# Optimization experiments

Hardware: AMD Instinct MI355X
Metric: run time of the kernel (lower is better)

The kernel has to match this reference:

```python
import jax, jax.numpy as jnp
import numpy as np

# ---- db6 filter bank (pywt conventions) ----
_REC_LO = np.array([0.11154074335008017, 0.4946238903983854, 0.7511339080215775,
                    0.3152503517092432, -0.22626469396516913, -0.12976686756709563,
                    0.09750160558707936, 0.02752286553001629, -0.031582039318031156,
                    0.0005538422009938016, 0.004777257511010651, -0.00107730108499558],
                   dtype=np.float32)
_REC_HI = _REC_LO[::-1].copy(); _REC_HI[1::2] *= -1.0          # qmf(rec_lo)
_DEC_LO = _REC_LO[::-1].copy()
_DEC_HI = _REC_HI[::-1].copy()
L = 12          # filter length
LEVEL = 8       # J
# pytorch_wavelets cross-correlates with dec[::-1] == true conv with dec.
# lax.conv_general_dilated is correlation, so analysis kernels = dec[::-1] = rec filters.
ANA = jnp.asarray(np.stack([_REC_LO, _REC_HI])[:, None, :])     # [2,1,L]
SYN = jnp.asarray(np.stack([_DEC_LO, _DEC_HI])[None, :, :])     # [1,2,L]


def dwt1d(x, J):
    """Multi-level DWT, mode='symmetric'. x: [B,C,N] -> (yl [B,C,m], [yh1..yhJ])."""
    B, C, N = x.shape
    lo = x.reshape(B * C, 1, N)
    highs = []
    for _ in range(J):
        n = lo.shape[-1]
        outlen = (n + L - 1) // 2                    # pywt dwt_coeff_len
        p = 2 * (outlen - 1) - n + L
        xp = jnp.pad(lo, ((0, 0), (0, 0), (p // 2, (p + 1) // 2)), mode='symmetric')
        y = jax.lax.conv_general_dilated(xp, ANA, (2,), 'VALID',
                                         dimension_numbers=('NCH', 'OIH', 'NCH'))
        lo = y[:, :1]
        highs.append(y[:, 1:].reshape(B, C, outlen))
    return lo.reshape(B, C, -1), highs


def idwt1d(yl, yhs):
    """Inverse of dwt1d. yl: [B,C,m], yhs list (level1..levelJ)."""
    B, C, _ = yl.shape
    lo = yl.reshape(B * C, 1, -1)
    pad = L - 1 - (L - 2)                            # torch convT padding L-2 -> lax pad 1
    for h in yhs[::-1]:
        h = h.reshape(B * C, 1, -1)
        if lo.shape[-1] > h.shape[-1]:               # 'unpad' extra sample
            lo = lo[..., :h.shape[-1]]
        xh = jnp.concatenate([lo, h], axis=1)        # [BC,2,n]
        lo = jax.lax.conv_general_dilated(xh, SYN, (1,), [(pad, pad)],
                                          lhs_dilation=(2,),
                                          dimension_numbers=('NCH', 'OIH', 'NCH'))
    return lo.reshape(B, C, -1)


def wno_forward(x, fc0_w, fc0_b, w1, w2, cw, cb, fc1_w, fc1_b, fc2_w, fc2_b):
    B, s, _ = x.shape
    grid = jnp.broadcast_to(jnp.linspace(0.0, 1.0, s, dtype=x.dtype)[None, :, None], (B, s, 1))
    v = jnp.concatenate([x, grid], axis=-1) @ fc0_w + fc0_b     # [B,s,W]
    v = v.transpose(0, 2, 1)                                     # [B,W,s]
    n_layers = w1.shape[0]
    for i in range(n_layers):
        yl, yhs = dwt1d(v, LEVEL)
        yl = jnp.einsum('bix,iox->box', yl, w1[i])               # mix approx coeffs
        yhs[-1] = jnp.einsum('bix,iox->box', yhs[-1], w2[i])     # mix finest-level detail
        x1 = idwt1d(yl, yhs)
        x2 = jnp.einsum('bis,io->bos', v, cw[i]) + cb[i][None, :, None]  # 1x1 conv
        v = x1 + x2
        if i < n_layers - 1:
            v = jax.nn.gelu(v, approximate=False)
    v = v.transpose(0, 2, 1)
    v = jax.nn.gelu(v @ fc1_w + fc1_b, approximate=False)
    return v @ fc2_w + fc2_b                                     # [B,s,1]


def setup_inputs() -> dict:
    key = jax.random.key(0)
    B, S, W, NL = 32, 8192, 64, 4
    n = S
    for _ in range(LEVEL):
        n = (n + L - 1) // 2
    modes = n                                                    # 42
    ks = jax.random.split(key, 12)
    scale = 1.0 / (W * W)
    return {
        'x': jax.random.normal(ks[0], (B, S, 1), jnp.float32),
        'fc0_w': jax.random.normal(ks[1], (2, W), jnp.float32) * 0.5,
        'fc0_b': jax.random.normal(ks[2], (W,), jnp.float32) * 0.1,
        'w1': scale * jax.random.uniform(ks[3], (NL, W, W, modes), jnp.float32),
        'w2': scale * jax.random.uniform(ks[4], (NL, W, W, modes), jnp.float32),
        'cw': jax.random.normal(ks[5], (NL, W, W), jnp.float32) * (1.0 / np.sqrt(W)),
        'cb': jax.random.normal(ks[6], (NL, W), jnp.float32) * 0.05,
        'fc1_w': jax.random.normal(ks[7], (W, 128), jnp.float32) * (1.0 / np.sqrt(W)),
        'fc1_b': jax.random.normal(ks[8], (128,), jnp.float32) * 0.05,
        'fc2_w': jax.random.normal(ks[9], (128, 1), jnp.float32) * (1.0 / np.sqrt(128.0)),
        'fc2_b': jax.random.normal(ks[10], (1,), jnp.float32) * 0.05,
    }


def reference(x, fc0_w, fc0_b, w1, w2, cw, cb, fc1_w, fc1_b, fc2_w, fc2_b):
    return wno_forward(x, fc0_w, fc0_b, w1, w2, cw, cb, fc1_w, fc1_b, fc2_w, fc2_b)
```

## Files before the change

kernel.cpp:

```cpp
#include <hip/hip_runtime.h>
#include <cmath>

#define BC 2048
#define S_LEN 8192
#define MODES 42
#define HTOT 8248
#define LO_STR 1036

static constexpr float C_LO[12] = {
  0.11154074335008017f, 0.4946238903983854f, 0.7511339080215775f,
  0.3152503517092432f, -0.22626469396516913f, -0.12976686756709563f,
  0.09750160558707936f, 0.02752286553001629f, -0.031582039318031156f,
  0.0005538422009938016f, 0.004777257511010651f, -0.00107730108499558f };

__device__ __forceinline__ float rec_lo_c(int k){ return C_LO[k]; }
__device__ __forceinline__ float rec_hi_c(int k){ float v = C_LO[11-k]; return (k&1)? -v : v; }
__device__ __forceinline__ float dec_lo_c(int k){ return C_LO[11-k]; }
__device__ __forceinline__ float dec_hi_c(int k){ float v = C_LO[k];    return (k&1)?  v : -v; }

__device__ __forceinline__ float erf_fast(float x){
  float ax = fabsf(x);
  float t  = __fdividef(1.0f, 1.0f + 0.3275911f * ax);
  float p  = ((((1.061405429f * t - 1.453152027f) * t) + 1.421413741f) * t - 0.284496736f) * t + 0.254829592f;
  float y  = 1.0f - p * t * __expf(-ax * ax);
  return copysignf(y, x);
}
__device__ __forceinline__ float gelu_f(float x){
  return 0.5f * x * (1.0f + erf_fast(x * 0.70710678118654752440f));
}

__device__ __forceinline__ int reflect_i(int t, int n){
  t = (t < 0) ? (-1 - t) : t;
  t = (t >= n) ? (2 * n - 1 - t) : t;
  return t;
}

__device__ __forceinline__ unsigned short bf16_rn(float x){
  unsigned int b = __float_as_uint(x);
  b += 0x7FFF + ((b >> 16) & 1);
  return (unsigned short)(b >> 16);
}
__device__ __forceinline__ float bf16_to_f(unsigned short h){
  return __uint_as_float(((unsigned int)h) << 16);
}

typedef short  v8s __attribute__((ext_vector_type(8)));
typedef float  v4f __attribute__((ext_vector_type(4)));
typedef unsigned short u16;

__device__ __forceinline__ void ld3f4(float* w, const float* s){
  *(float4*)&w[0] = *(const float4*)&s[0];
  *(float4*)&w[4] = *(const float4*)&s[4];
  *(float4*)&w[8] = *(const float4*)&s[8];
}
__device__ __forceinline__ void ld5f4(float* w, const float* s){
  *(float4*)&w[0]  = *(const float4*)&s[0];
  *(float4*)&w[4]  = *(const float4*)&s[4];
  *(float4*)&w[8]  = *(const float4*)&s[8];
  *(float4*)&w[12] = *(const float4*)&s[12];
  *(float4*)&w[16] = *(const float4*)&s[16];
}
__device__ __forceinline__ void ld4f2(float* w, const float* s){
  *(float2*)&w[0] = *(const float2*)&s[0];
  *(float2*)&w[2] = *(const float2*)&s[2];
  *(float2*)&w[4] = *(const float2*)&s[4];
  *(float2*)&w[6] = *(const float2*)&s[6];
}

__device__ __forceinline__ void stage_g(float* dst, const float* src, int g0, int cnt, int n){
  for (int j4 = threadIdx.x; j4 < (cnt >> 2); j4 += 256) {
    int g = g0 + 4 * j4;
    float4 val;
    if (g >= 0 && g + 3 < n) val = *(const float4*)&src[g];
    else {
      val.x = (g   >= 0 && g   < n) ? src[g]   : 0.f;
      val.y = (g+1 >= 0 && g+1 < n) ? src[g+1] : 0.f;
      val.z = (g+2 >= 0 && g+2 < n) ? src[g+2] : 0.f;
      val.w = (g+3 >= 0 && g+3 < n) ? src[g+3] : 0.f;
    }
    *(float4*)&dst[4*j4] = val;
  }
}

__device__ __forceinline__ void stage_band4(float* dst, const float* src, int len, int alloc){
  for (int i4 = threadIdx.x; i4 < (alloc >> 2); i4 += 256) {
    int i = 4 * i4;
    float4 v;
    if (i + 3 < len) v = *(const float4*)&src[i];
    else {
      v.x = (i   < len) ? src[i]   : 0.f;
      v.y = (i+1 < len) ? src[i+1] : 0.f;
      v.z = (i+2 < len) ? src[i+2] : 0.f;
      v.w = (i+3 < len) ? src[i+3] : 0.f;
    }
    *(float4*)&dst[i] = v;
  }
}

template<int SH>
__device__ __forceinline__ void idwt4s(const float* wl, const float* wh, float* o4){
  #pragma unroll
  for (int d = 0; d < 4; ++d) {
    const int q = SH + (d >> 1);
    float acc = 0.f;
    if (d & 1) {
      #pragma unroll
      for (int i = 0; i < 6; ++i) acc += wl[q+i]*dec_lo_c(2*i)   + wh[q+i]*dec_hi_c(2*i);
    } else {
      #pragma unroll
      for (int i = 0; i < 6; ++i) acc += wl[q+i]*dec_lo_c(2*i+1) + wh[q+i]*dec_hi_c(2*i+1);
    }
    o4[d] = acc;
  }
}

__global__ __launch_bounds__(256) void prep_split(
    const float* __restrict__ fc1w, const float* __restrict__ cw,
    u16* __restrict__ whH, u16* __restrict__ whL,
    u16* __restrict__ wcH, u16* __restrict__ wcL)
{
  int i = blockIdx.x * 256 + threadIdx.x;
  if (i < 8192) {
    int c = i >> 7, j = i & 127;
    float wv = fc1w[i];
    u16 h = bf16_rn(wv);
    float lo = wv - bf16_to_f(h);
    int cs = c ^ ((j & 7) << 3);
    whH[j * 64 + cs] = h; whL[j * 64 + cs] = bf16_rn(lo);
  }
  int k = i - 8192;
  if (k >= 0 && k < 16384) {
    int l = k >> 12, r = k & 4095;
    int c = r >> 6, o = r & 63;
    float wv = cw[k];
    u16 h = bf16_rn(wv);
    float lo = wv - bf16_to_f(h);
    int cs = c ^ ((o & 7) << 3);
    wcH[l * 4096 + o * 64 + cs] = h; wcL[l * 4096 + o * 64 + cs] = bf16_rn(lo);
  }
}

__global__ __launch_bounds__(256) void fc0_kernel(
    const float* __restrict__ x, const float* __restrict__ w,
    const float* __restrict__ bias, float* __restrict__ v)
{
  int p = blockIdx.x * 256 + threadIdx.x;
  int b = p >> 13, s = p & 8191;
  float xv = x[p];
  float g  = (float)s * (1.0f / 8191.0f);
  for (int c = 0; c < 64; ++c) {
    v[((size_t)(b * 64 + c)) * S_LEN + s] = xv * w[c] + g * w[64 + c] + bias[c];
  }
}

__global__ __launch_bounds__(256) void dwt_big(
    const float* __restrict__ vin, float* __restrict__ highs, float* __restrict__ lo_f)
{
  __shared__ alignas(16) float sVE[1096], sVO[1096];
  __shared__ alignas(16) float sL1Eb[548], sL1Ob[548];
  __shared__ alignas(16) float sL2E[276], sL2O[276];
  float* sL1E = sL1Eb + 4;
  float* sL1O = sL1Ob + 4;

  int seq = blockIdx.x >> 2, c = blockIdx.x & 3;
  const float* src = vin + (size_t)seq * S_LEN;
  float* hseq = highs + (size_t)seq * HTOT;
  int tid = threadIdx.x;

  int g0 = 2080 * c - 76;
  for (int j4 = tid; j4 < 545; j4 += 256) {
    int g = g0 + 4 * j4;
    float4 val;
    if (g >= 0 && g + 3 < 8192) val = *(const float4*)&src[g];
    else {
      val.x = src[reflect_i(g,   8192)];
      val.y = src[reflect_i(g+1, 8192)];
      val.z = src[reflect_i(g+2, 8192)];
      val.w = src[reflect_i(g+3, 8192)];
    }
    *(float2*)&sVE[2*j4] = make_float2(val.x, val.z);
    *(float2*)&sVO[2*j4] = make_float2(val.y, val.w);
  }
  __syncthreads();

  {
    int base1m = 1040 * c - 32;
    int uh1 = (c < 3) ? 1072 : 1013;
    for (int u0 = 4 * tid; u0 < 1084; u0 += 1024) {
      float we[12], wo[12];
      ld3f4(we, &sVE[u0]); ld3f4(wo, &sVO[u0]);
      float lo4[4], hi4[4];
      #pragma unroll
      for (int d = 0; d < 4; ++d) {
        float alo = 0.f, ahi = 0.f;
        #pragma unroll
        for (int j = 0; j < 6; ++j) {
          float e = we[d+1+j], oo = wo[d+1+j];
          alo += e * rec_lo_c(2*j) + oo * rec_lo_c(2*j+1);
          ahi += e * rec_hi_c(2*j) + oo * rec_hi_c(2*j+1);
        }
        lo4[d] = alo; hi4[d] = ahi;
      }
      *(float2*)&sL1E[u0 >> 1] = make_float2(lo4[0], lo4[2]);
      *(float2*)&sL1O[u0 >> 1] = make_float2(lo4[1], lo4[3]);
      if (u0 >= 32 && u0 + 3 < uh1) {
        *(float4*)&hseq[base1m + u0] = make_float4(hi4[0], hi4[1], hi4[2], hi4[3]);
      } else {
        #pragma unroll
        for (int d = 0; d < 4; ++d) {
          int u = u0 + d;
          if (u >= 32 && u < uh1) hseq[base1m + u] = hi4[d];
        }
      }
    }
  }
  __syncthreads();
  if (c == 0) {
    for (int u = tid; u < 32; u += 256) {
      int j = 63 - u;
      float v = (j & 1) ? sL1O[j >> 1] : sL1E[j >> 1];
      if (u & 1) sL1O[u >> 1] = v; else sL1E[u >> 1] = v;
    }
  }
  if (c == 3) {
    for (int u = 1013 + tid; u < 1084; u += 256) {
      int j = 2025 - u;
      float v = (j & 1) ? sL1O[j >> 1] : sL1E[j >> 1];
      if (u & 1) sL1O[u >> 1] = v; else sL1E[u >> 1] = v;
    }
  }
  __syncthreads();

  {
    int base2m = 520 * c - 12;
    int uh2 = (c < 3) ? 532 : 508;
    for (int u0 = 4 * tid; u0 < 536; u0 += 1024) {
      float we[12], wo[12];
      ld3f4(we, &sL1E[u0 - 4]); ld3f4(wo, &sL1O[u0 - 4]);
      float lo4[4], hi4[4];
      #pragma unroll
      for (int d = 0; d < 4; ++d) {
        float alo = 0.f, ahi = 0.f;
        #pragma unroll
        for (int j = 0; j < 6; ++j) {
          float e = we[d+3+j], oo = wo[d+3+j];
          alo += e * rec_lo_c(2*j) + oo * rec_lo_c(2*j+1);
          ahi += e * rec_hi_c(2*j) + oo * rec_hi_c(2*j+1);
        }
        lo4[d] = alo; hi4[d] = ahi;
      }
      *(float2*)&sL2E[u0 >> 1] = make_float2(lo4[0], lo4[2]);
      *(float2*)&sL2O[u0 >> 1] = make_float2(lo4[1], lo4[3]);
      if (u0 >= 12 && u0 < uh2)
        *(float4*)&hseq[4104 + base2m + u0] = make_float4(hi4[0], hi4[1], hi4[2], hi4[3]);
    }
  }
  __syncthreads();
  if (c == 0) {
    for (int u = tid; u < 12; u += 256) {
      int j = 23 - u;
      float v = (j & 1) ? sL2O[j >> 1] : sL2E[j >> 1];
      if (u & 1) sL2O[u >> 1] = v; else sL2E[u >> 1] = v;
    }
  }
  if (c == 3) {
    for (int u = 508 + tid; u < 536; u += 256) {
      int j = 1015 - u;
      float v = (j & 1) ? sL2O[j >> 1] : sL2E[j >> 1];
      if (u & 1) sL2O[u >> 1] = v; else sL2E[u >> 1] = v;
    }
  }
  __syncthreads();

  for (int u0 = 4 * tid; u0 < 260; u0 += 1024) {
    float we[12], wo[12];
    ld3f4(we, &sL2E[u0]); ld3f4(wo, &sL2O[u0]);
    float lo4[4], hi4[4];
    #pragma unroll
    for (int d = 0; d < 4; ++d) {
      float alo = 0.f, ahi = 0.f;
      #pragma unroll
      for (int j = 0; j < 6; ++j) {
        float e = we[d+1+j], oo = wo[d+1+j];
        alo += e * rec_lo_c(2*j) + oo * rec_lo_c(2*j+1);
        ahi += e * rec_hi_c(2*j) + oo * rec_hi_c(2*j+1);
      }
      lo4[d] = alo; hi4[d] = ahi;
    }
    int m0 = 260 * c + u0;
    if (m0 + 3 < 1033) {
      *(float4*)&lo_f[(size_t)seq * LO_STR + m0] = make_float4(lo4[0], lo4[1], lo4[2], lo4[3]);
      *(float4*)&hseq[6160 + m0] = make_float4(hi4[0], hi4[1], hi4[2], hi4[3]);
    } else {
      #pragma unroll
      for (int d = 0; d < 4; ++d) {
        int m = m0 + d;
        if (m < 1033 && u0 + d < 260) {
          lo_f[(size_t)seq * LO_STR + m] = lo4[d];
          hseq[6160 + m] = hi4[d];
        }
      }
    }
  }
}

__device__ __forceinline__ void dwt_lvl_v(const float* in, int n, float* out, int outn, float* hg)
{
  for (int u0 = 4*(int)threadIdx.x; u0 < outn; u0 += 1024) {
    bool fast = (u0 >= 8) && (2*u0 + 7 < n) && (u0 + 3 < outn);
    if (fast) {
      float w[20];
      ld5f4(w, &in[2*u0 - 12]);
      #pragma unroll
      for (int d = 0; d < 4; ++d) {
        float alo = 0.f, ahi = 0.f;
        #pragma unroll
        for (int k = 0; k < 12; ++k) {
          float x = w[2*d + 2 + k];
          alo += x * rec_lo_c(k); ahi += x * rec_hi_c(k);
        }
        out[u0+d] = alo; hg[u0+d] = ahi;
      }
    } else {
      for (int d = 0; d < 4; ++d) {
        if (u0 + d < outn) {
          float alo = 0.f, ahi = 0.f;
          #pragma unroll
          for (int k = 0; k < 12; ++k) {
            float x = in[reflect_i(2*(u0+d) + k - 10, n)];
            alo += x * rec_lo_c(k); ahi += x * rec_hi_c(k);
          }
          out[u0+d] = alo; hg[u0+d] = ahi;
        }
      }
    }
  }
  __syncthreads();
}

__global__ __launch_bounds__(256) void dwt_small(
    const float* __restrict__ lo_f, float* __restrict__ highs, float* __restrict__ yl)
{
  __shared__ alignas(16) float A[1040], Bb[528];
  int seq = blockIdx.x;
  const float* src = lo_f + (size_t)seq * LO_STR;
  float* hseq = highs + (size_t)seq * HTOT;
  for (int i = 4*(int)threadIdx.x; i < 1033; i += 1024) {
    if (i + 3 < 1033) *(float4*)&A[i] = *(const float4*)&src[i];
    else { for (int d = 0; d < 4; ++d) if (i + d < 1033) A[i+d] = src[i+d]; }
  }
  __syncthreads();
  dwt_lvl_v(A, 1033, Bb, 522, hseq + 7196);
  dwt_lvl_v(Bb, 522, A, 266, hseq + 7720);
  dwt_lvl_v(A, 266, Bb, 138, hseq + 7988);
  dwt_lvl_v(Bb, 138, A, 74,  hseq + 8128);
  dwt_lvl_v(A, 74,  Bb, 42,  hseq + 8204);
  for (int m = threadIdx.x; m < MODES; m += 256) yl[seq * MODES + m] = Bb[m];
}

__device__ __forceinline__ void idwt_lvl4(const float* lo, const float* h, float* out, int outn)
{
  for (int u0 = 4*(int)threadIdx.x; u0 < outn; u0 += 1024) {
    int q = u0 >> 1;
    float wl[8], wh[8];
    ld4f2(wl, &lo[q]); ld4f2(wh, &h[q]);
    float o4[4]; idwt4s<0>(wl, wh, o4);
    if (u0 + 3 < outn) *(float4*)&out[u0] = make_float4(o4[0], o4[1], o4[2], o4[3]);
    else { for (int d = 0; d < 4; ++d) if (u0 + d < outn) out[u0+d] = o4[d]; }
  }
  __syncthreads();
}

__global__ __launch_bounds__(256) void idwt_small(
    const float* __restrict__ yl_raw, const float* __restrict__ highs,
    const float* __restrict__ w1l, const float* __restrict__ w2l,
    float* __restrict__ lo_i)
{
  __shared__ alignas(16) float bands[1120], wa[272], wb[528];
  int seq = blockIdx.x;
  int b = seq >> 6, o = seq & 63;
  const float* hseq = highs + (size_t)seq * HTOT;
  int t = threadIdx.x;

  stage_band4(bands + 96,  hseq + 8128, 74, 80);
  stage_band4(bands + 176, hseq + 7988, 138, 144);
  stage_band4(bands + 320, hseq + 7720, 266, 272);
  stage_band4(bands + 592, hseq + 7196, 522, 528);

  if (t >= 42 && t < 48) { bands[t] = 0.f; bands[48 + t] = 0.f; }
  if (t < 42) {
    const float* yr = yl_raw + (size_t)b * 2688 + t;
    const float* hh = highs + (size_t)(b * 64) * HTOT + 8204 + t;
    const float* wl = w1l + o * 42 + t;
    const float* wh = w2l + o * 42 + t;
    float accl = 0.f, acch = 0.f;
    #pragma unroll 4
    for (int i = 0; i < 64; ++i) {
      accl += yr[i * 42] * wl[i * 2688];
      acch += hh[(size_t)i * HTOT] * wh[i * 2688];
    }
    bands[t] = accl; bands[48 + t] = acch;
  }
  __syncthreads();

  idwt_lvl4(bands + 0,   bands + 48,  wa, 74);
  idwt_lvl4(wa,          bands + 96,  wb, 138);
  idwt_lvl4(wb,          bands + 176, wa, 266);
  idwt_lvl4(wa,          bands + 320, wb, 522);

  for (int u0 = 4 * t; u0 < 1033; u0 += 1024) {
    int q = u0 >> 1;
    float wl[8], wh[8];
    ld4f2(wl, &wb[q]); ld4f2(wh, &bands[592 + q]);
    float o4[4]; idwt4s<0>(wl, wh, o4);
    float* dst = lo_i + (size_t)seq * LO_STR + u0;
    if (u0 + 3 < 1033) *(float4*)&dst[0] = make_float4(o4[0], o4[1], o4[2], o4[3]);
    else { for (int d = 0; d < 4; ++d) if (u0 + d < 1033) dst[d] = o4[d]; }
  }
}

__global__ __launch_bounds__(256) void idwt_big(
    const float* __restrict__ lo_i, const float* __restrict__ highs, float* __restrict__ x1)
{
  __shared__ alignas(16) float sL3[288], sH3[288], sL2[544], sH2[544], sL1[1048], sH1[1048];
  int seq = blockIdx.x >> 2, c = blockIdx.x & 3;
  const float* hseq = highs + (size_t)seq * HTOT;
  const float* l3   = lo_i + (size_t)seq * LO_STR;
  int g3 = 256*c - 4, g2 = 512*c - 4, g1 = 1024*c - 4;
  int t = threadIdx.x;

  stage_g(sL3, l3,          g3, 288, 1033);
  stage_g(sH3, hseq + 6160, g3, 288, 1033);
  stage_g(sH2, hseq + 4104, g2, 544, 2056);
  stage_g(sH1, hseq,        g1, 1048, 4101);
  __syncthreads();

  for (int u0 = 4 * t; u0 < 536; u0 += 1024) {
    int q = u0 >> 1;
    float wl[8], wh[8];
    ld4f2(wl, &sL3[q + 2]); ld4f2(wh, &sH3[q + 2]);
    float o4[4]; idwt4s<1>(wl, wh, o4);
    #pragma unroll
    for (int d = 0; d < 4; ++d) {
      int m = 512*c - 2 + u0 + d;
      o4[d] = (m >= 0 && m < 2056) ? o4[d] : 0.f;
    }
    *(float2*)&sL2[u0 + 2] = make_float2(o4[0], o4[1]);
    *(float2*)&sL2[u0 + 4] = make_float2(o4[2], o4[3]);
  }
  __syncthreads();

  for (int u0 = 4 * t; u0 < 1040; u0 += 1024) {
    int q = u0 >> 1;
    float wl[8], wh[8];
    ld4f2(wl, &sL2[q + 2]); ld4f2(wh, &sH2[q + 2]);
    float o4[4]; idwt4s<1>(wl, wh, o4);
    #pragma unroll
    for (int d = 0; d < 4; ++d) {
      int m = 1024*c - 2 + u0 + d;
      o4[d] = (m >= 0 && m < 4101) ? o4[d] : 0.f;
    }
    *(float2*)&sL1[u0 + 2] = make_float2(o4[0], o4[1]);
    *(float2*)&sL1[u0 + 4] = make_float2(o4[2], o4[3]);
  }
  __syncthreads();

  for (int u0 = 4 * t; u0 < 2048; u0 += 1024) {
    int q = u0 >> 1;
    float wl[8], wh[8];
    ld4f2(wl, &sL1[q + 4]); ld4f2(wh, &sH1[q + 4]);
    float o4[4]; idwt4s<0>(wl, wh, o4);
    *(float4*)&x1[(size_t)seq * S_LEN + 2048*c + u0] = make_float4(o4[0], o4[1], o4[2], o4[3]);
  }
}

__global__ __launch_bounds__(256) void pw_mfma(
    const float* __restrict__ x1, float* v,
    const u16* __restrict__ wcH, const u16* __restrict__ wcL,
    const float* __restrict__ cb, int do_gelu)
{
  __shared__ u16 aH[64][64], aL[64][64];
  __shared__ u16 wH[64][64], wL[64][64];
  __shared__ float cbl[64];
  int b  = blockIdx.x >> 7;
  int s0 = (blockIdx.x & 127) << 6;
  int t  = threadIdx.x;

  {
    const v8s* srcH = (const v8s*)wcH;
    const v8s* srcL = (const v8s*)wcL;
    v8s* dstH = (v8s*)&wH[0][0];
    v8s* dstL = (v8s*)&wL[0][0];
    #pragma unroll
    for (int r = 0; r < 2; ++r) {
      dstH[t + 256 * r] = srcH[t + 256 * r];
      dstL[t + 256 * r] = srcL[t + 256 * r];
    }
  }
  if (t < 64) cbl[t] = cb[t];

  #pragma unroll
  for (int r = 0; r < 4; ++r) {
    int idx = t + 256 * r;
    int ch = idx >> 4, p4 = (idx & 15) << 2;
    float4 xv = *(const float4*)&v[((size_t)(b * 64 + ch)) * S_LEN + s0 + p4];
    u16 h0 = bf16_rn(xv.x); aH[p4+0][ch ^ (((p4+0)&7)<<3)] = h0; aL[p4+0][ch ^ (((p4+0)&7)<<3)] = bf16_rn(xv.x - bf16_to_f(h0));
    u16 h1 = bf16_rn(xv.y); aH[p4+1][ch ^ (((p4+1)&7)<<3)] = h1; aL[p4+1][ch ^ (((p4+1)&7)<<3)] = bf16_rn(xv.y - bf16_to_f(h1));
    u16 h2 = bf16_rn(xv.z); aH[p4+2][ch ^ (((p4+2)&7)<<3)] = h2; aL[p4+2][ch ^ (((p4+2)&7)<<3)] = bf16_rn(xv.z - bf16_to_f(h2));
    u16 h3 = bf16_rn(xv.w); aH[p4+3][ch ^ (((p4+3)&7)<<3)] = h3; aL[p4+3][ch ^ (((p4+3)&7)<<3)] = bf16_rn(xv.w - bf16_to_f(h3));
  }
  __syncthreads();

  int l = t & 63, wv_ = t >> 6;
  int pi = l & 15, kg = l >> 4;
  int pos = wv_ * 16 + pi;
  int swz = (pi & 7) << 3;

  v4f acc[4];
  #pragma unroll
  for (int i = 0; i < 4; ++i) acc[i] = v4f{0.f, 0.f, 0.f, 0.f};

  #pragma unroll
  for (int kt = 0; kt < 2; ++kt) {
    int ka = (kg * 8 + kt * 32) ^ swz;
    v8s ah = *(const v8s*)&aH[pos][ka];
    v8s al = *(const v8s*)&aL[pos][ka];
    #pragma unroll
    for (int ct = 0; ct < 4; ++ct) {
      int o = ct * 16 + pi;
      v8s bh = *(const v8s*)&wH[o][ka];
      v8s bl = *(const v8s*)&wL[o][ka];
      acc[ct] = __builtin_amdgcn_mfma_f32_16x16x32_bf16(ah, bh, acc[ct], 0, 0, 0);
      acc[ct] = __builtin_amdgcn_mfma_f32_16x16x32_bf16(ah, bl, acc[ct], 0, 0, 0);
      acc[ct] = __builtin_amdgcn_mfma_f32_16x16x32_bf16(al, bh, acc[ct], 0, 0, 0);
    }
  }

  #pragma unroll
  for (int ct = 0; ct < 4; ++ct) {
    int o = ct * 16 + pi;
    size_t base = ((size_t)(b * 64 + o)) * S_LEN + s0 + wv_ * 16 + kg * 4;
    float4 x4 = *(const float4*)&x1[base];
    float cbv = cbl[o];
    float y0 = acc[ct][0] + x4.x + cbv;
    float y1 = acc[ct][1] + x4.y + cbv;
    float y2 = acc[ct][2] + x4.z + cbv;
    float y3 = acc[ct][3] + x4.w + cbv;
    if (do_gelu) { y0 = gelu_f(y0); y1 = gelu_f(y1); y2 = gelu_f(y2); y3 = gelu_f(y3); }
    float4 y4 = make_float4(y0, y1, y2, y3);
    *(float4*)&v[base] = y4;
  }
}

__global__ __launch_bounds__(256) void head_mfma(
    const float* __restrict__ v,
    const u16* __restrict__ whH, const u16* __restrict__ whL,
    const float* __restrict__ fc1b, const float* __restrict__ fc2w,
    const float* __restrict__ fc2b, float* __restrict__ out)
{
  __shared__ u16 aH[64][64], aL[64][64];
  __shared__ u16 wH[128][64], wL[128][64];
  __shared__ float f1b[128], f2w[128];
  int b  = blockIdx.x >> 7;
  int s0 = (blockIdx.x & 127) << 6;
  int t  = threadIdx.x;

  {
    const v8s* srcH = (const v8s*)whH;
    const v8s* srcL = (const v8s*)whL;
    v8s* dstH = (v8s*)&wH[0][0];
    v8s* dstL = (v8s*)&wL[0][0];
    #pragma unroll
    for (int r = 0; r < 4; ++r) {
      dstH[t + 256 * r] = srcH[t + 256 * r];
      dstL[t + 256 * r] = srcL[t + 256 * r];
    }
  }
  if (t < 128) { f1b[t] = fc1b[t]; f2w[t] = fc2w[t]; }

  #pragma unroll
  for (int r = 0; r < 4; ++r) {
    int idx = t + 256 * r;
    int ch = idx >> 4, p4 = (idx & 15) << 2;
    float4 xv = *(const float4*)&v[((size_t)(b * 64 + ch)) * S_LEN + s0 + p4];
    u16 h0 = bf16_rn(xv.x); aH[p4+0][ch ^ (((p4+0)&7)<<3)] = h0; aL[p4+0][ch ^ (((p4+0)&7)<<3)] = bf16_rn(xv.x - bf16_to_f(h0));
    u16 h1 = bf16_rn(xv.y); aH[p4+1][ch ^ (((p4+1)&7)<<3)] = h1; aL[p4+1][ch ^ (((p4+1)&7)<<3)] = bf16_rn(xv.y - bf16_to_f(h1));
    u16 h2 = bf16_rn(xv.z); aH[p4+2][ch ^ (((p4+2)&7)<<3)] = h2; aL[p4+2][ch ^ (((p4+2)&7)<<3)] = bf16_rn(xv.z - bf16_to_f(h2));
    u16 h3 = bf16_rn(xv.w); aH[p4+3][ch ^ (((p4+3)&7)<<3)] = h3; aL[p4+3][ch ^ (((p4+3)&7)<<3)] = bf16_rn(xv.w - bf16_to_f(h3));
  }
  __syncthreads();

  int l = t & 63, wv_ = t >> 6;
  int pi = l & 15, kg = l >> 4;
  int pos = wv_ * 16 + pi;
  int swz = (pi & 7) << 3;

  v4f acc[8];
  #pragma unroll
  for (int i = 0; i < 8; ++i) acc[i] = v4f{0.f, 0.f, 0.f, 0.f};

  #pragma unroll
  for (int kt = 0; kt < 2; ++kt) {
    int ka = (kg * 8 + kt * 32) ^ swz;
    v8s ah = *(const v8s*)&aH[pos][ka];
    v8s al = *(const v8s*)&aL[pos][ka];
    #pragma unroll
    for (int ct = 0; ct < 8; ++ct) {
      int j = ct * 16 + pi;
      v8s bh = *(const v8s*)&wH[j][ka];
      v8s bl = *(const v8s*)&wL[j][ka];
      acc[ct] = __builtin_amdgcn_mfma_f32_16x16x32_bf16(ah, bh, acc[ct], 0, 0, 0);
      acc[ct] = __builtin_amdgcn_mfma_f32_16x16x32_bf16(ah, bl, acc[ct], 0, 0, 0);
      acc[ct] = __builtin_amdgcn_mfma_f32_16x16x32_bf16(al, bh, acc[ct], 0, 0, 0);
    }
  }

  float part[4] = {0.f, 0.f, 0.f, 0.f};
  #pragma unroll
  for (int ct = 0; ct < 8; ++ct) {
    int j = ct * 16 + pi;
    float bias = f1b[j], f2 = f2w[j];
    #pragma unroll
    for (int r = 0; r < 4; ++r) {
      float d = acc[ct][r] + bias;
      part[r] += f2 * gelu_f(d);
    }
  }
  #pragma unroll
  for (int r = 0; r < 4; ++r) {
    part[r] += __shfl_xor(part[r], 1, 16);
    part[r] += __shfl_xor(part[r], 2, 16);
    part[r] += __shfl_xor(part[r], 4, 16);
    part[r] += __shfl_xor(part[r], 8, 16);
  }
  if (pi == 0) {
    float b2 = fc2b[0];
    float4 o4 = make_float4(part[0] + b2, part[1] + b2, part[2] + b2, part[3] + b2);
    *(float4*)&out[(size_t)b * S_LEN + s0 + wv_ * 16 + kg * 4] = o4;
  }
}

extern "C" void kernel_launch(void* const* d_in, const int* in_sizes, int n_in,
                              void* d_out, int out_size, void* d_ws, size_t ws_size,
                              hipStream_t stream) {
  const float* x    = (const float*)d_in[0];
  const float* fc0w = (const float*)d_in[1];
  const float* fc0b = (const float*)d_in[2];
  const float* w1   = (const float*)d_in[3];
  const float* w2   = (const float*)d_in[4];
  const float* cw   = (const float*)d_in[5];
  const float* cb   = (const float*)d_in[6];
  const float* fc1w = (const float*)d_in[7];
  const float* fc1b = (const float*)d_in[8];
  const float* fc2w = (const float*)d_in[9];
  const float* fc2b = (const float*)d_in[10];
  float* out = (float*)d_out;

  float* ws     = (float*)d_ws;
  float* v      = ws;
  float* x1     = v      + (size_t)BC * S_LEN;
  float* highs  = x1     + (size_t)BC * S_LEN;
  float* yl_raw = highs  + (size_t)BC * HTOT;
  float* lo_f   = yl_raw + (size_t)BC * MODES;
  float* lo_i   = lo_f   + (size_t)BC * LO_STR;
  u16*   whH    = (u16*)(lo_i + (size_t)BC * LO_STR);
  u16*   whL    = whH + 8192;
  u16*   wcH    = whL + 8192;
  u16*   wcL    = wcH + 16384;
  size_t needed = (size_t)((char*)(wcL + 16384) - (char*)ws);
  if (ws_size < needed) return;

  prep_split<<<96, 256, 0, stream>>>(fc1w, cw, whH, whL, wcH, wcL);
  fc0_kernel<<<1024, 256, 0, stream>>>(x, fc0w, fc0b, v);

  for (int i = 0; i < 4; ++i) {
    const float* w1l = w1 + (size_t)i * 64 * 64 * MODES;
    const float* w2l = w2 + (size_t)i * 64 * 64 * MODES;
    dwt_big<<<BC * 4, 256, 0, stream>>>(v, highs, lo_f);
    dwt_small<<<BC, 256, 0, stream>>>(lo_f, highs, yl_raw);
    idwt_small<<<BC, 256, 0, stream>>>(yl_raw, highs, w1l, w2l, lo_i);
    idwt_big<<<BC * 4, 256, 0, stream>>>(lo_i, highs, x1);
    pw_mfma<<<4096, 256, 0, stream>>>(x1, v, wcH + i * 4096, wcL + i * 4096, cb + i * 64, (i < 3) ? 1 : 0);
  }

  head_mfma<<<4096, 256, 0, stream>>>(v, whH, whL, fc1b, fc2w, fc2b, out);
}
```

Baseline: 584.6 us.

## Pack four sequences per block in small DWT/IDWT kernels; vectorize fc0

dwt_small and idwt_small now give each 64-thread wavefront its own sequence, with per-sub shared buffers, so one 256-thread block handles four sequences. Before, most threads sat idle on the short coarse levels. fc0 is rewritten so each thread writes one float4 for one channel, replacing the strided 64-channel loop per thread with coalesced vector stores. Shared memory per block grows fourfold, which may limit occupancy, and block-wide __syncthreads still couples the four wavefronts.

Result: no change. 591.9 us (+1.3%).

```diff
diff --git a/kernel.cpp b/kernel.cpp
--- a/kernel.cpp
+++ b/kernel.cpp
@@ -82,8 +82,8 @@
   }
 }
 
-__device__ __forceinline__ void stage_band4(float* dst, const float* src, int len, int alloc){
-  for (int i4 = threadIdx.x; i4 < (alloc >> 2); i4 += 256) {
+__device__ __forceinline__ void stage_band4_64(float* dst, const float* src, int len, int alloc, int t64){
+  for (int i4 = t64; i4 < (alloc >> 2); i4 += 64) {
     int i = 4 * i4;
     float4 v;
     if (i + 3 < len) v = *(const float4*)&src[i];
@@ -145,12 +145,18 @@
     const float* __restrict__ bias, float* __restrict__ v)
 {
   int p = blockIdx.x * 256 + threadIdx.x;
-  int b = p >> 13, s = p & 8191;
-  float xv = x[p];
-  float g  = (float)s * (1.0f / 8191.0f);
-  for (int c = 0; c < 64; ++c) {
-    v[((size_t)(b * 64 + c)) * S_LEN + s] = xv * w[c] + g * w[64 + c] + bias[c];
-  }
+  int s4 = (p & 2047) << 2;
+  int c  = (p >> 11) & 63;
+  int b  = p >> 17;
+  float4 xv = *(const float4*)&x[b * S_LEN + s4];
+  float w0 = w[c], w1v = w[64 + c], bc = bias[c];
+  const float inv = 1.0f / 8191.0f;
+  float4 o;
+  o.x = xv.x * w0 + (float)(s4    ) * inv * w1v + bc;
+  o.y = xv.y * w0 + (float)(s4 + 1) * inv * w1v + bc;
+  o.z = xv.z * w0 + (float)(s4 + 2) * inv * w1v + bc;
+  o.w = xv.w * w0 + (float)(s4 + 3) * inv * w1v + bc;
+  *(float4*)&v[((size_t)(b * 64 + c)) * S_LEN + s4] = o;
 }
 
 __global__ __launch_bounds__(256) void dwt_big(
@@ -304,9 +310,9 @@
   }
 }
 
-__device__ __forceinline__ void dwt_lvl_v(const float* in, int n, float* out, int outn, float* hg)
-{
-  for (int u0 = 4*(int)threadIdx.x; u0 < outn; u0 += 1024) {
+__device__ __forceinline__ void dwt_lvl_v64(const float* in, int n, float* out, int outn, float* hg, int t64)
+{
+  for (int u0 = 4*t64; u0 < outn; u0 += 256) {
     bool fast = (u0 >= 8) && (2*u0 + 7 < n) && (u0 + 3 < outn);
     if (fast) {
       float w[20];
@@ -341,26 +347,29 @@
 __global__ __launch_bounds__(256) void dwt_small(
     const float* __restrict__ lo_f, float* __restrict__ highs, float* __restrict__ yl)
 {
-  __shared__ alignas(16) float A[1040], Bb[528];
-  int seq = blockIdx.x;
+  __shared__ alignas(16) float A[4][1040], Bb[4][528];
+  int sub = threadIdx.x >> 6, t64 = threadIdx.x & 63;
+  int seq = blockIdx.x * 4 + sub;
   const float* src = lo_f + (size_t)seq * LO_STR;
   float* hseq = highs + (size_t)seq * HTOT;
-  for (int i = 4*(int)threadIdx.x; i < 1033; i += 1024) {
-    if (i + 3 < 1033) *(float4*)&A[i] = *(const float4*)&src[i];
-    else { for (int d = 0; d < 4; ++d) if (i + d < 1033) A[i+d] = src[i+d]; }
-  }
-  __syncthreads();
-  dwt_lvl_v(A, 1033, Bb, 522, hseq + 7196);
-  dwt_lvl_v(Bb, 522, A, 266, hseq + 7720);
-  dwt_lvl_v(A, 266, Bb, 138, hseq + 7988);
-  dwt_lvl_v(Bb, 138, A, 74,  hseq + 8128);
-  dwt_lvl_v(A, 74,  Bb, 42,  hseq + 8204);
-  for (int m = threadIdx.x; m < MODES; m += 256) yl[seq * MODES + m] = Bb[m];
-}
-
-__device__ __forceinline__ void idwt_lvl4(const float* lo, const float* h, float* out, int outn)
-{
-  for (int u0 = 4*(int)threadIdx.x; u0 < outn; u0 += 1024) {
+  float* As = A[sub];
+  float* Bs = Bb[sub];
+  for (int i = 4*t64; i < 1033; i += 256) {
+    if (i + 3 < 1033) *(float4*)&As[i] = *(const float4*)&src[i];
+    else { for (int d = 0; d < 4; ++d) if (i + d < 1033) As[i+d] = src[i+d]; }
+  }
+  __syncthreads();
+  dwt_lvl_v64(As, 1033, Bs, 522, hseq + 7196, t64);
+  dwt_lvl_v64(Bs, 522, As, 266, hseq + 7720, t64);
+  dwt_lvl_v64(As, 266, Bs, 138, hseq + 7988, t64);
+  dwt_lvl_v64(Bs, 138, As, 74,  hseq + 8128, t64);
+  dwt_lvl_v64(As, 74,  Bs, 42,  hseq + 8204, t64);
+  for (int m = t64; m < MODES; m += 64) yl[seq * MODES + m] = Bs[m];
+}
+
+__device__ __forceinline__ void idwt_lvl4_64(const float* lo, const float* h, float* out, int outn, int t64)
+{
+  for (int u0 = 4*t64; u0 < outn; u0 += 256) {
     int q = u0 >> 1;
     float wl[8], wh[8];
     ld4f2(wl, &lo[q]); ld4f2(wh, &h[q]);
@@ -376,42 +385,45 @@
     const float* __restrict__ w1l, const float* __restrict__ w2l,
     float* __restrict__ lo_i)
 {
-  __shared__ alignas(16) float bands[1120], wa[272], wb[528];
-  int seq = blockIdx.x;
+  __shared__ alignas(16) float bands[4][1120], wa[4][272], wb[4][528];
+  int sub = threadIdx.x >> 6, t64 = threadIdx.x & 63;
+  int seq = blockIdx.x * 4 + sub;
   int b = seq >> 6, o = seq & 63;
   const float* hseq = highs + (size_t)seq * HTOT;
-  int t = threadIdx.x;
-
-  stage_band4(bands + 96,  hseq + 8128, 74, 80);
-  stage_band4(bands + 176, hseq + 7988, 138, 144);
-  stage_band4(bands + 320, hseq + 7720, 266, 272);
-  stage_band4(bands + 592, hseq + 7196, 522, 528);
-
-  if (t >= 42 && t < 48) { bands[t] = 0.f; bands[48 + t] = 0.f; }
-  if (t < 42) {
-    const float* yr = yl_raw + (size_t)b * 2688 + t;
-    const float* hh = highs + (size_t)(b * 64) * HTOT + 8204 + t;
-    const float* wl = w1l + o * 42 + t;
-    const float* wh = w2l + o * 42 + t;
+  float* bs = bands[sub];
+  float* was = wa[sub];
+  float* wbs = wb[sub];
+
+  stage_band4_64(bs + 96,  hseq + 8128, 74, 80, t64);
+  stage_band4_64(bs + 176, hseq + 7988, 138, 144, t64);
+  stage_band4_64(bs + 320, hseq + 7720, 266, 272, t64);
+  stage_band4_64(bs + 592, hseq + 7196, 522, 528, t64);
+
+  if (t64 >= 42 && t64 < 48) { bs[t64] = 0.f; bs[48 + t64] = 0.f; }
+  if (t64 < 42) {
+    const float* yr = yl_raw + (size_t)b * 2688 + t64;
+    const float* hh = highs + (size_t)(b * 64) * HTOT + 8204 + t64;
+    const float* wl = w1l + o * 42 + t64;
+    const float* wh = w2l + o * 42 + t64;
     float accl = 0.f, acch = 0.f;
     #pragma unroll 4
     for (int i = 0; i < 64; ++i) {
       accl += yr[i * 42] * wl[i * 2688];
       acch += hh[(size_t)i * HTOT] * wh[i * 2688];
     }
-    bands[t] = accl; bands[48 + t] = acch;
-  }
-  __syncthreads();
-
-  idwt_lvl4(bands + 0,   bands + 48,  wa, 74);
-  idwt_lvl4(wa,          bands + 96,  wb, 138);
-  idwt_lvl4(wb,          bands + 176, wa, 266);
-  idwt_lvl4(wa,          bands + 320, wb, 522);
-
-  for (int u0 = 4 * t; u0 < 1033; u0 += 1024) {
+    bs[t64] = accl; bs[48 + t64] = acch;
+  }
+  __syncthreads();
+
+  idwt_lvl4_64(bs + 0,   bs + 48,  was, 74, t64);
+  idwt_lvl4_64(was,      bs + 96,  wbs, 138, t64);
+  idwt_lvl4_64(wbs,      bs + 176, was, 266, t64);
+  idwt_lvl4_64(was,      bs + 320, wbs, 522, t64);
+
+  for (int u0 = 4 * t64; u0 < 1033; u0 += 256) {
     int q = u0 >> 1;
     float wl[8], wh[8];
-    ld4f2(wl, &wb[q]); ld4f2(wh, &bands[592 + q]);
+    ld4f2(wl, &wbs[q]); ld4f2(wh, &bs[592 + q]);
     float o4[4]; idwt4s<0>(wl, wh, o4);
     float* dst = lo_i + (size_t)seq * LO_STR + u0;
     if (u0 + 3 < 1033) *(float4*)&dst[0] = make_float4(o4[0], o4[1], o4[2], o4[3]);
@@ -671,14 +683,14 @@
   if (ws_size < needed) return;
 
   prep_split<<<96, 256, 0, stream>>>(fc1w, cw, whH, whL, wcH, wcL);
-  fc0_kernel<<<1024, 256, 0, stream>>>(x, fc0w, fc0b, v);
+  fc0_kernel<<<16384, 256, 0, stream>>>(x, fc0w, fc0b, v);
 
   for (int i = 0; i < 4; ++i) {
     const float* w1l = w1 + (size_t)i * 64 * 64 * MODES;
     const float* w2l = w2 + (size_t)i * 64 * 64 * MODES;
     dwt_big<<<BC * 4, 256, 0, stream>>>(v, highs, lo_f);
-    dwt_small<<<BC, 256, 0, stream>>>(lo_f, highs, yl_raw);
-    idwt_small<<<BC, 256, 0, stream>>>(yl_raw, highs, w1l, w2l, lo_i);
+    dwt_small<<<BC / 4, 256, 0, stream>>>(lo_f, highs, yl_raw);
+    idwt_small<<<BC / 4, 256, 0, stream>>>(yl_raw, highs, w1l, w2l, lo_i);
     idwt_big<<<BC * 4, 256, 0, stream>>>(lo_i, highs, x1);
     pw_mfma<<<4096, 256, 0, stream>>>(x1, v, wcH + i * 4096, wcL + i * 4096, cb + i * 64, (i < 3) ? 1 : 0);
   }
```
